# Kernel tuning notes

Hardware: AMD Instinct MI355X
Metric: run time of the kernel (lower is better)

Reference implementation:

```python
import jax, jax.numpy as jnp
import numpy as np

HIDDEN = 2048
N_HEADS = 16
N_KV = 2
HEAD_DIM = 256
PARTIAL = 0.25
ROT = int(HEAD_DIM * PARTIAL)  # 64
BATCH, SEQ = 1, 4096
NEG = -1e9


def apply_partial_rope(x, cos, sin):
    # x: (b, s, h, d); rotate first ROT dims (rotate-half convention), pass rest through.
    x_rot, x_pass = x[..., :ROT], x[..., ROT:]
    half = ROT // 2
    x1, x2 = x_rot[..., :half], x_rot[..., half:]
    c = cos[None, :, None, :]  # (1, s, 1, rot/2)
    s = sin[None, :, None, :]
    rotated = jnp.concatenate([x1 * c - x2 * s, x1 * s + x2 * c], axis=-1)
    return jnp.concatenate([rotated, x_pass], axis=-1)


def setup_inputs() -> dict:
    key = jax.random.key(0)
    ks = jax.random.split(key, 6)
    hidden_states = jax.random.normal(ks[0], (BATCH, SEQ, HIDDEN), dtype=jnp.float32)
    # RoPE tables: theta = 10000^{-2i/rot}
    inv_freq = 1.0 / (10000.0 ** (np.arange(0, ROT, 2, dtype=np.float32) / ROT))
    ang = np.arange(SEQ, dtype=np.float32)[:, None] * inv_freq[None, :]  # (s, rot/2)
    cos = jnp.asarray(np.cos(ang))
    sin = jnp.asarray(np.sin(ang))
    # causal mask (1,1,s,s)
    mask = jnp.triu(jnp.full((SEQ, SEQ), NEG, dtype=jnp.float32), k=1)[None, None]
    scale = 0.02
    wq = jax.random.normal(ks[1], (HIDDEN, N_HEADS * HEAD_DIM), dtype=jnp.float32) * scale
    wk = jax.random.normal(ks[2], (HIDDEN, N_KV * HEAD_DIM), dtype=jnp.float32) * scale
    wv = jax.random.normal(ks[3], (HIDDEN, N_KV * HEAD_DIM), dtype=jnp.float32) * scale
    wo = jax.random.normal(ks[4], (N_HEADS * HEAD_DIM, HIDDEN), dtype=jnp.float32) * scale
    return {"hidden_states": hidden_states, "cos": cos, "sin": sin,
            "attention_mask": mask, "wq": wq, "wk": wk, "wv": wv, "wo": wo}


def reference(hidden_states, cos, sin, attention_mask, wq, wk, wv, wo):
    b, s, _ = hidden_states.shape
    g = N_HEADS // N_KV
    scale = HEAD_DIM ** -0.5
    q = (hidden_states @ wq).reshape(b, s, N_HEADS, HEAD_DIM)
    k = (hidden_states @ wk).reshape(b, s, N_KV, HEAD_DIM)
    v = (hidden_states @ wv).reshape(b, s, N_KV, HEAD_DIM)
    q = apply_partial_rope(q, cos, sin)
    k = apply_partial_rope(k, cos, sin)
    new_k, new_v = k, v  # kv cache (no prior cache)
    # GQA without repeat_interleave: group q heads by their kv head.
    # repeat_interleave maps q head h -> kv head h // g, matching this reshape.
    qg = q.reshape(b, s, N_KV, g, HEAD_DIM)
    scores = jnp.einsum('bqkgd,blkd->bkgql', qg, k) * scale  # (b, kv, g, s, s)
    scores = scores + attention_mask[:, :, None]  # broadcast (b,1,1,s,s)
    probs = jax.nn.softmax(scores.astype(jnp.float32), axis=-1).astype(q.dtype)
    ctx = jnp.einsum('bkgql,blkd->bqkgd', probs, v)  # (b, s, kv, g, d)
    attn_out = ctx.reshape(b, s, N_HEADS * HEAD_DIM)
    output = attn_out @ wo
    return output, new_k, new_v
```

## Files before the change

### kernel.cpp

```cpp
#include <hip/hip_runtime.h>
#include <hip/hip_bf16.h>

typedef __bf16 bf16;
typedef bf16 bf16x8 __attribute__((ext_vector_type(8)));
typedef bf16 bf16x4 __attribute__((ext_vector_type(4)));
typedef float f32x4 __attribute__((ext_vector_type(4)));

#define SEQ    4096
#define HIDDEN 2048
#define NHEADS 16
#define NKV    2
#define HDIM   256
#define ROTD   64
#define ROTH   32
#define QN     (NHEADS*HDIM)
#define KVN    (NKV*HDIM)

typedef __attribute__((address_space(3))) unsigned int lds_u32;
typedef const __attribute__((address_space(1))) unsigned int glb_u32;
__device__ __forceinline__ void async_copy16(const void* g, void* l) {
  __builtin_amdgcn_global_load_lds((glb_u32*)g, (lds_u32*)l, 16, 0, 0);
}

__global__ __launch_bounds__(256) void convert_f32_bf16(
    const float* __restrict__ in, bf16* __restrict__ out, int n)
{
  int i = (blockIdx.x * 256 + threadIdx.x) * 4;
  if (i >= n) return;
  f32x4 v = *(const f32x4*)(in + i);
  bf16x4 o;
  #pragma unroll
  for (int j = 0; j < 4; j++) o[j] = (bf16)v[j];
  *(bf16x4*)(out + i) = o;
}

template<typename T>
__global__ __launch_bounds__(256) void transpose_to_bf16(
    const T* __restrict__ in, bf16* __restrict__ out, int R, int C)
{
  __shared__ float tile[32][33];
  int bx = blockIdx.x * 32;
  int by = blockIdx.y * 32;
  int tx = threadIdx.x & 31, ty = threadIdx.x >> 5;
  #pragma unroll
  for (int i = 0; i < 4; i++)
    tile[ty + i*8][tx] = (float)in[(size_t)(by + ty + i*8) * C + bx + tx];
  __syncthreads();
  #pragma unroll
  for (int i = 0; i < 4; i++)
    out[(size_t)(bx + ty + i*8) * R + by + tx] = (bf16)tile[tx][ty + i*8];
}

template<bool WF32, bool WBF16>
__global__ __launch_bounds__(256) void gemm_bt(
    const bf16* __restrict__ A, const bf16* __restrict__ Bt,
    float* __restrict__ Cf, bf16* __restrict__ Cb,
    int M, int N, int K)
{
  const int bm = blockIdx.y * 128;
  const int bn = blockIdx.x * 128;
  const int tid = threadIdx.x;
  const int wave = tid >> 6, lane = tid & 63;
  const int l16 = lane & 15, quad = lane >> 4;
  const int wr = (wave & 1) * 64;
  const int wc = (wave >> 1) * 64;

  __shared__ bf16 As[128*32];
  __shared__ bf16 Bs[128*32];

  f32x4 acc[4][4];
  #pragma unroll
  for (int r = 0; r < 4; r++)
    #pragma unroll
    for (int c = 0; c < 4; c++) acc[r][c] = (f32x4){0.f,0.f,0.f,0.f};

  const int arow = tid >> 2;
  const int acol = (tid & 3) * 8;
  const bf16* ag0 = A  + (size_t)(bm + arow)      * K + acol;
  const bf16* ag1 = A  + (size_t)(bm + 64 + arow) * K + acol;
  const bf16* bg0 = Bt + (size_t)(bn + arow)      * K + acol;
  const bf16* bg1 = Bt + (size_t)(bn + 64 + arow) * K + acol;
  bf16* la = As + tid*8;
  bf16* lb = Bs + tid*8;

  for (int kk = 0; kk < K; kk += 32) {
    __syncthreads();
    async_copy16(ag0 + kk, la);
    async_copy16(ag1 + kk, la + 2048);
    async_copy16(bg0 + kk, lb);
    async_copy16(bg1 + kk, lb + 2048);
    __syncthreads();

    bf16x8 af[4], bfr[4];
    #pragma unroll
    for (int r = 0; r < 4; r++) af[r]  = *(const bf16x8*)&As[(wr + r*16 + l16)*32 + quad*8];
    #pragma unroll
    for (int c = 0; c < 4; c++) bfr[c] = *(const bf16x8*)&Bs[(wc + c*16 + l16)*32 + quad*8];
    #pragma unroll
    for (int r = 0; r < 4; r++)
      #pragma unroll
      for (int c = 0; c < 4; c++)
        acc[r][c] = __builtin_amdgcn_mfma_f32_16x16x32_bf16(af[r], bfr[c], acc[r][c], 0, 0, 0);
  }

  #pragma unroll
  for (int r = 0; r < 4; r++)
    #pragma unroll
    for (int c = 0; c < 4; c++)
      #pragma unroll
      for (int rr = 0; rr < 4; rr++) {
        size_t idx = (size_t)(bm + wr + r*16 + quad*4 + rr) * N + bn + wc + c*16 + l16;
        if (WF32)  Cf[idx] = acc[r][c][rr];
        if (WBF16) Cb[idx] = (bf16)acc[r][c][rr];
      }
}

#define G256_STG(gp, stride, lbase, b, h, kt) do {                            \
    async_copy16((gp) + (size_t)((h)*128     ) * (stride) + (size_t)(kt)*64,  \
                 (lbase) + (b)*16384 + (h)*8192);                             \
    async_copy16((gp) + (size_t)((h)*128 + 64) * (stride) + (size_t)(kt)*64,  \
                 (lbase) + (b)*16384 + (h)*8192 + 4096);                      \
  } while (0)

#define G256_DSA(b, P) do {                                                   \
    _Pragma("unroll")                                                         \
    for (int m2 = 0; m2 < 2; m2++) {                                          \
      const int ro = (b)*16384 + arow0 + ((P)*2 + m2) * 1024;                 \
      af[m2][0] = *(const bf16x8*)&smem[ro + fc0];                            \
      af[m2][1] = *(const bf16x8*)&smem[ro + fc1];                            \
    }                                                                         \
  } while (0)

#define G256_DSB(b) do {                                                      \
    _Pragma("unroll")                                                         \
    for (int n4 = 0; n4 < 4; n4++) {                                          \
      const int ro = 32768 + (b)*16384 + brow0 + n4 * 1024;                   \
      bq[n4][0] = *(const bf16x8*)&smem[ro + fc0];                            \
      bq[n4][1] = *(const bf16x8*)&smem[ro + fc1];                            \
    }                                                                         \
  } while (0)

#define G256_MM(P) do {                                                       \
    _Pragma("unroll")                                                         \
    for (int m2 = 0; m2 < 2; m2++)                                            \
      _Pragma("unroll")                                                       \
      for (int n4 = 0; n4 < 4; n4++) {                                        \
        acc[(P)*2+m2][n4] = __builtin_amdgcn_mfma_f32_16x16x32_bf16(          \
            af[m2][0], bq[n4][0], acc[(P)*2+m2][n4], 0, 0, 0);                \
        acc[(P)*2+m2][n4] = __builtin_amdgcn_mfma_f32_16x16x32_bf16(          \
            af[m2][1], bq[n4][1], acc[(P)*2+m2][n4], 0, 0, 0);                \
      }                                                                       \
  } while (0)

#define G256_BAR  __builtin_amdgcn_s_barrier()
#define G256_WLG  do { asm volatile("s_waitcnt lgkmcnt(0)" ::: "memory");     \
                       __builtin_amdgcn_sched_barrier(0); } while (0)

template<bool WF32, bool WBF16>
__global__ __launch_bounds__(512, 2) void gemm256(
    const bf16* __restrict__ A, const bf16* __restrict__ Bt,
    float* __restrict__ Cf0, float* __restrict__ Cf1, bf16* __restrict__ Cb,
    int N, int K, int lda, int ldb)
{
  const int gx = gridDim.x;
  const int nwg = gx * gridDim.y;
  int wg = blockIdx.y * gx + blockIdx.x;
  wg = (wg & 7) * (nwg >> 3) + (wg >> 3);
  const int bn = (wg % gx) * 256;
  const int bm = (wg / gx) * 256;

  const int z = blockIdx.z;
  A  += (size_t)z * K;
  Bt += (size_t)z * K;
  float* __restrict__ Cf = z ? Cf1 : Cf0;

  const int tid = threadIdx.x;
  const int lane = tid & 63;
  const int l16 = lane & 15, quad = lane >> 4;
  const int wv = tid >> 6;
  const int wm = wv >> 2;
  const int wn = wv & 3;

  __shared__ bf16 smem[65536];

  const int srow = tid >> 3;
  const int scol = ((tid & 7) ^ (srow & 7)) << 3;
  const bf16* Ag = A  + (size_t)(bm + srow) * lda + scol;
  const bf16* Bg = Bt + (size_t)(bn + srow) * ldb + scol;
  bf16* lA = smem + tid * 8;
  bf16* lB = smem + 32768 + tid * 8;

  const int fsw = l16 & 7;
  const int fc0 = ((quad       ^ fsw) << 3);
  const int fc1 = (((4 + quad) ^ fsw) << 3);
  const int arow0 = (wm * 128 + l16) * 64;
  const int brow0 = (wn * 64  + l16) * 64;

  f32x4 acc[8][4];
  #pragma unroll
  for (int m = 0; m < 8; m++)
    #pragma unroll
    for (int n = 0; n < 4; n++) acc[m][n] = (f32x4){0.f,0.f,0.f,0.f};

  const int niter = K >> 7;

  G256_STG(Ag, lda, lA, 0, 0, 0);  G256_STG(Ag, lda, lA, 0, 1, 0);
  G256_STG(Bg, ldb, lB, 0, 0, 0);  G256_STG(Bg, ldb, lB, 0, 1, 0);
  G256_STG(Bg, ldb, lB, 1, 0, 1);  G256_STG(Bg, ldb, lB, 1, 1, 1);
  asm volatile("s_waitcnt vmcnt(4)" ::: "memory");
  G256_BAR;

  bf16x8 af[2][2];
  bf16x8 bq[4][2];

  for (int i = 0; i < niter; i++) {
    const int O = 2*i + 1;
    const bool nl = (i + 1 < niter);

    G256_DSB(0); G256_DSA(0, 0);
    G256_STG(Ag, lda, lA, 1, 0, O);
    G256_BAR; G256_WLG;
    __builtin_amdgcn_s_setprio(1); G256_MM(0); __builtin_amdgcn_s_setprio(0);
    G256_BAR;
    G256_DSA(0, 1);
    G256_STG(Ag, lda, lA, 1, 1, O);
    G256_BAR; G256_WLG;
    __builtin_amdgcn_s_setprio(1); G256_MM(1); __builtin_amdgcn_s_setprio(0);
    G256_BAR;
    G256_DSA(0, 2);
    if (nl) G256_STG(Bg, ldb, lB, 0, 0, O+1);
    G256_BAR; G256_WLG;
    __builtin_amdgcn_s_setprio(1); G256_MM(2); __builtin_amdgcn_s_setprio(0);
    G256_BAR;
    G256_DSA(0, 3);
    if (nl) G256_STG(Bg, ldb, lB, 0, 1, O+1);
    G256_BAR; G256_WLG;
    __builtin_amdgcn_s_setprio(1); G256_MM(3); __builtin_amdgcn_s_setprio(0);
    if (nl) asm volatile("s_waitcnt vmcnt(4)" ::: "memory");
    else    asm volatile("s_waitcnt vmcnt(0)" ::: "memory");
    G256_BAR;
    G256_DSB(1); G256_DSA(1, 0);
    if (nl) G256_STG(Ag, lda, lA, 0, 0, O+1);
    G256_BAR; G256_WLG;
    __builtin_amdgcn_s_setprio(1); G256_MM(0); __builtin_amdgcn_s_setprio(0);
    G256_BAR;
    G256_DSA(1, 1);
    if (nl) G256_STG(Ag, lda, lA, 0, 1, O+1);
    G256_BAR; G256_WLG;
    __builtin_amdgcn_s_setprio(1); G256_MM(1); __builtin_amdgcn_s_setprio(0);
    G256_BAR;
    G256_DSA(1, 2);
    if (nl) G256_STG(Bg, ldb, lB, 1, 0, O+2);
    G256_BAR; G256_WLG;
    __builtin_amdgcn_s_setprio(1); G256_MM(2); __builtin_amdgcn_s_setprio(0);
    G256_BAR;
    G256_DSA(1, 3);
    if (nl) G256_STG(Bg, ldb, lB, 1, 1, O+2);
    G256_BAR; G256_WLG;
    __builtin_amdgcn_s_setprio(1); G256_MM(3); __builtin_amdgcn_s_setprio(0);
    if (nl) asm volatile("s_waitcnt vmcnt(4)" ::: "memory");
    G256_BAR;
  }

  #pragma unroll
  for (int mf = 0; mf < 8; mf++)
    #pragma unroll
    for (int n = 0; n < 4; n++)
      #pragma unroll
      for (int rr = 0; rr < 4; rr++) {
        size_t idx = (size_t)(bm + wm*128 + mf*16 + quad*4 + rr) * N
                   + bn + wn*64 + n*16 + l16;
        if (WF32)  Cf[idx] = acc[mf][n][rr];
        if (WBF16) Cb[idx] = (bf16)acc[mf][n][rr];
      }
}

__global__ __launch_bounds__(256) void add_f32(
    const float* __restrict__ a, float* __restrict__ b, int n)
{
  int i = (blockIdx.x * 256 + threadIdx.x) * 4;
  if (i >= n) return;
  f32x4 x = *(const f32x4*)(a + i);
  f32x4 y = *(const f32x4*)(b + i);
  #pragma unroll
  for (int j = 0; j < 4; j++) y[j] += x[j];
  *(f32x4*)(b + i) = y;
}

__global__ __launch_bounds__(256) void rope_kernel(
    bf16* __restrict__ Q, bf16* __restrict__ K,
    const float* __restrict__ cosb, const float* __restrict__ sinb,
    float* __restrict__ newk)
{
  int s = blockIdx.x;
  int t = threadIdx.x;
  __shared__ float cf[ROTH], sf[ROTH];
  if (t < ROTH) { cf[t] = cosb[s*ROTH + t]; sf[t] = sinb[s*ROTH + t]; }
  __syncthreads();

  float qv[4];
  #pragma unroll
  for (int i = 0; i < 4; i++) {
    int w = t + 256*i;
    int h = w >> 6, d = w & 63;
    size_t base = ((size_t)s*NHEADS + h)*HDIM;
    if (d < ROTH) {
      float x1 = (float)Q[base + d], x2 = (float)Q[base + d + ROTH];
      qv[i] = x1*cf[d] - x2*sf[d];
    } else {
      int dd = d - ROTH;
      float x1 = (float)Q[base + dd], x2 = (float)Q[base + d];
      qv[i] = x1*sf[dd] + x2*cf[dd];
    }
  }
  float kvv[2];
  #pragma unroll
  for (int i = 0; i < 2; i++) {
    int w = t + 256*i;
    int h = w >> 8, d = w & 255;
    size_t base = ((size_t)s*NKV + h)*HDIM;
    if (d < ROTH) {
      kvv[i] = (float)K[base + d]*cf[d] - (float)K[base + d + ROTH]*sf[d];
    } else if (d < ROTD) {
      int dd = d - ROTH;
      kvv[i] = (float)K[base + dd]*sf[dd] + (float)K[base + d]*cf[dd];
    } else {
      kvv[i] = (float)K[base + d];
    }
  }
  __syncthreads();
  #pragma unroll
  for (int i = 0; i < 4; i++) {
    int w = t + 256*i;
    int h = w >> 6, d = w & 63;
    Q[((size_t)s*NHEADS + h)*HDIM + d] = (bf16)qv[i];
  }
  #pragma unroll
  for (int i = 0; i < 2; i++) {
    int w = t + 256*i;
    int h = w >> 8, d = w & 255;
    size_t base = ((size_t)s*NKV + h)*HDIM;
    K[base + d]    = (bf16)kvv[i];
    newk[base + d] = kvv[i];
  }
}

__global__ __launch_bounds__(256, 2) void attn_v5(
    const bf16* __restrict__ Q, const bf16* __restrict__ Kc,
    const bf16* __restrict__ Vt, bf16* __restrict__ ctx)
{
  const int h = blockIdx.y, kvh = h >> 3;
  const int qs = (int)(gridDim.x - 1 - blockIdx.x);
  const int tid = threadIdx.x, wave = tid >> 6, lane = tid & 63;
  const int l16 = lane & 15, quad = lane >> 4;
  const int q0 = qs*128 + wave*32;

  __shared__ bf16 Ks[32*256];
  __shared__ bf16 Vs[256*32];
  __shared__ bf16 PsAll[4][32][40];
  bf16 (*Ps)[40] = PsAll[wave];

  bf16x8 aq[2][8];
  #pragma unroll
  for (int u = 0; u < 2; u++) {
    const bf16* qp = Q + (size_t)(q0 + u*16 + l16)*QN + h*HDIM + quad*8;
    #pragma unroll
    for (int c = 0; c < 8; c++) aq[u][c] = *(const bf16x8*)(qp + c*32);
  }

  f32x4 o[2][16];
  #pragma unroll
  for (int u = 0; u < 2; u++)
    #pragma unroll
    for (int c = 0; c < 16; c++) o[u][c] = (f32x4){0.f,0.f,0.f,0.f};
  float lsum[2][4] = {{0.f,0.f,0.f,0.f},{0.f,0.f,0.f,0.f}};

  const int krow0 = tid >> 5;
  const int kcg   = ((tid & 31) ^ (krow0 & 7)) * 8;
  const bf16* kg  = Kc + (size_t)kvh*HDIM + kcg;
  const int vd0 = tid >> 2;
  const int vcg = ((tid & 3) ^ (vd0 & 3)) * 8;
  const bf16* vg  = Vt + (size_t)(kvh*HDIM + vd0)*SEQ + vcg;
  bf16* ksl = Ks + tid*8;
  bf16* vsl = Vs + tid*8;

  const int ntiles = qs*4 + 4;
  for (int t = 0; t < ntiles; t++) {
    const int l0 = t*32;
    __syncthreads();
    #pragma unroll
    for (int p = 0; p < 4; p++) {
      async_copy16(kg + (size_t)(l0 + p*8 + krow0)*KVN, ksl + p*2048);
      async_copy16(vg + (size_t)(p*64)*SEQ + l0,        vsl + p*2048);
    }
    __syncthreads();

    if (l0 > q0 + 31) continue;

    f32x4 s[2][2];
    #pragma unroll
    for (int u = 0; u < 2; u++)
      #pragma unroll
      for (int t4 = 0; t4 < 2; t4++) s[u][t4] = (f32x4){0.f,0.f,0.f,0.f};
    #pragma unroll
    for (int c = 0; c < 8; c++) {
      const int cs = ((c*4 + quad) ^ (l16 & 7)) * 8;
      #pragma unroll
      for (int t4 = 0; t4 < 2; t4++) {
        bf16x8 kb = *(const bf16x8*)&Ks[(t4*16 + l16)*256 + cs];
        #pragma unroll
        for (int u = 0; u < 2; u++)
          s[u][t4] = __builtin_amdgcn_mfma_f32_16x16x32_bf16(aq[u][c], kb, s[u][t4], 0, 0, 0);
      }
    }

    const bool need_mask = (l0 + 31 > q0);
    #pragma unroll
    for (int u = 0; u < 2; u++)
      #pragma unroll
      for (int r = 0; r < 4; r++) {
        const int row = q0 + u*16 + quad*4 + r;
        float p0 = __expf(fmaf(s[u][0][r], 0.0625f, -12.0f));
        float p1 = __expf(fmaf(s[u][1][r], 0.0625f, -12.0f));
        if (need_mask) {
          if (l0 +      l16 > row) p0 = 0.f;
          if (l0 + 16 + l16 > row) p1 = 0.f;
        }
        lsum[u][r] += p0 + p1;
        Ps[u*16 + quad*4 + r][l16]      = (bf16)p0;
        Ps[u*16 + quad*4 + r][16 + l16] = (bf16)p1;
      }

    bf16x8 pa[2];
    #pragma unroll
    for (int u = 0; u < 2; u++) pa[u] = *(const bf16x8*)&Ps[u*16 + l16][quad*8];
    #pragma unroll
    for (int c = 0; c < 16; c++) {
      const int vs = ((quad ^ (l16 & 3))) * 8;
      bf16x8 vb = *(const bf16x8*)&Vs[(c*16 + l16)*32 + vs];
      #pragma unroll
      for (int u = 0; u < 2; u++)
        o[u][c] = __builtin_amdgcn_mfma_f32_16x16x32_bf16(pa[u], vb, o[u][c], 0, 0, 0);
    }
  }

  #pragma unroll
  for (int u = 0; u < 2; u++)
    #pragma unroll
    for (int r = 0; r < 4; r++) {
      float l = lsum[u][r];
      l += __shfl_xor(l, 1);
      l += __shfl_xor(l, 2);
      l += __shfl_xor(l, 4);
      l += __shfl_xor(l, 8);
      float inv = 1.0f / l;
      size_t base = (size_t)(q0 + u*16 + quad*4 + r)*QN + h*HDIM;
      #pragma unroll
      for (int c = 0; c < 16; c++)
        ctx[base + c*16 + l16] = (bf16)(o[u][c][r] * inv);
    }
}

extern "C" void kernel_launch(void* const* d_in, const int* in_sizes, int n_in,
                              void* d_out, int out_size, void* d_ws, size_t ws_size,
                              hipStream_t stream)
{
  const float* X    = (const float*)d_in[0];
  const float* cosb = (const float*)d_in[1];
  const float* sinb = (const float*)d_in[2];
  const float* wq   = (const float*)d_in[4];
  const float* wk   = (const float*)d_in[5];
  const float* wv   = (const float*)d_in[6];
  const float* wo   = (const float*)d_in[7];

  float* out  = (float*)d_out;
  float* newk = out  + (size_t)SEQ*HIDDEN;
  float* newv = newk + (size_t)SEQ*KVN;

  bf16* Xb  = (bf16*)d_ws;
  bf16* wqT = Xb  + (size_t)SEQ*HIDDEN;
  bf16* Qb  = wqT + (size_t)QN*HIDDEN;
  bf16* Kb  = Qb  + (size_t)SEQ*QN;
  bf16* Vb  = Kb  + (size_t)SEQ*KVN;
  bf16* Vt  = Vb  + (size_t)SEQ*KVN;
  bf16* wkT = Vt  + (size_t)KVN*SEQ;
  bf16* wvT = wkT + (size_t)KVN*HIDDEN;
  bf16* woT = wvT + (size_t)KVN*HIDDEN;
  bf16* ctx = Xb;
  float* part = (float*)Qb;

  dim3 blk(256);
  convert_f32_bf16<<<dim3(SEQ*HIDDEN/1024), blk, 0, stream>>>(X, Xb, SEQ*HIDDEN);
  transpose_to_bf16<float><<<dim3(QN/32,     HIDDEN/32), blk, 0, stream>>>(wq, wqT, HIDDEN, QN);
  transpose_to_bf16<float><<<dim3(KVN/32,    HIDDEN/32), blk, 0, stream>>>(wk, wkT, HIDDEN, KVN);
  transpose_to_bf16<float><<<dim3(KVN/32,    HIDDEN/32), blk, 0, stream>>>(wv, wvT, HIDDEN, KVN);
  transpose_to_bf16<float><<<dim3(HIDDEN/32, QN/32),     blk, 0, stream>>>(wo, woT, QN, HIDDEN);

  gemm256<false,true><<<dim3(QN/256, SEQ/256, 1), dim3(512), 0, stream>>>(
      Xb, wqT, nullptr, nullptr, Qb, QN, HIDDEN, HIDDEN, HIDDEN);
  gemm_bt<false,true><<<dim3(KVN/128, SEQ/128), blk, 0, stream>>>(Xb, wkT, nullptr, Kb, SEQ, KVN, HIDDEN);
  gemm_bt<true, true><<<dim3(KVN/128, SEQ/128), blk, 0, stream>>>(Xb, wvT, newv,   Vb, SEQ, KVN, HIDDEN);

  rope_kernel<<<dim3(SEQ), blk, 0, stream>>>(Qb, Kb, cosb, sinb, newk);
  transpose_to_bf16<bf16><<<dim3(KVN/32, SEQ/32), blk, 0, stream>>>(Vb, Vt, SEQ, KVN);

  attn_v5<<<dim3(SEQ/128, NHEADS), blk, 0, stream>>>(Qb, Kb, Vt, ctx);

  gemm256<true,false><<<dim3(HIDDEN/256, SEQ/256, 2), dim3(512), 0, stream>>>(
      ctx, woT, out, part, nullptr, HIDDEN, QN/2, QN, QN);
  add_f32<<<dim3(SEQ*HIDDEN/1024), blk, 0, stream>>>(part, out, SEQ*HIDDEN);
}
```

Measured before the change: 741.3 us.

## Double-buffer K/V tiles in attention and reorder blocks for load balance

The attention kernel now keeps two LDS buffers for K and V and prefetches tile t+2 while tile t is being computed. Explicit vmcnt waits and barriers replace the two per-tile __syncthreads, which hides global-to-LDS latency behind the MFMA work. Blocks are also remapped so the long causal q-blocks are scheduled first and paired with short ones across the two halves of the grid, to balance work. The cost is double the K/V LDS footprint, which may reduce occupancy, plus hand-counted waitcnt logic that has to match the number of outstanding loads.

Result: faster. 722.6 us (-2.5%).

```diff
diff --git a/kernel.cpp b/kernel.cpp
--- a/kernel.cpp
+++ b/kernel.cpp
@@ -345,18 +345,20 @@
   }
 }
 
-__global__ __launch_bounds__(256, 2) void attn_v5(
+__global__ __launch_bounds__(256, 2) void attn_v6(
     const bf16* __restrict__ Q, const bf16* __restrict__ Kc,
     const bf16* __restrict__ Vt, bf16* __restrict__ ctx)
 {
-  const int h = blockIdx.y, kvh = h >> 3;
-  const int qs = (int)(gridDim.x - 1 - blockIdx.x);
+  const int d = blockIdx.y * gridDim.x + blockIdx.x;
+  const int r = (d < 256) ? d : 767 - d;
+  const int qs = 31 - (r >> 4);
+  const int h  = r & 15, kvh = h >> 3;
   const int tid = threadIdx.x, wave = tid >> 6, lane = tid & 63;
   const int l16 = lane & 15, quad = lane >> 4;
   const int q0 = qs*128 + wave*32;
 
-  __shared__ bf16 Ks[32*256];
-  __shared__ bf16 Vs[256*32];
+  __shared__ bf16 Ks[2][32*256];
+  __shared__ bf16 Vs[2][256*32];
   __shared__ bf16 PsAll[4][32][40];
   bf16 (*Ps)[40] = PsAll[wave];
 
@@ -381,83 +383,104 @@
   const int vd0 = tid >> 2;
   const int vcg = ((tid & 3) ^ (vd0 & 3)) * 8;
   const bf16* vg  = Vt + (size_t)(kvh*HDIM + vd0)*SEQ + vcg;
-  bf16* ksl = Ks + tid*8;
-  bf16* vsl = Vs + tid*8;
 
   const int ntiles = qs*4 + 4;
+
+  #define ATTN_STAGE(t, b) do {                                               \
+    const int _l0 = (t)*32;                                                   \
+    bf16* _ks = &Ks[b][0] + tid*8;                                            \
+    bf16* _vs = &Vs[b][0] + tid*8;                                            \
+    _Pragma("unroll")                                                         \
+    for (int p = 0; p < 4; p++) {                                             \
+      async_copy16(kg + (size_t)(_l0 + p*8 + krow0)*KVN, _ks + p*2048);       \
+      async_copy16(vg + (size_t)(p*64)*SEQ + _l0,        _vs + p*2048);       \
+    }                                                                         \
+  } while (0)
+
+  ATTN_STAGE(0, 0);
+  ATTN_STAGE(1, 1);
+  asm volatile("s_waitcnt vmcnt(8)" ::: "memory");
+  __builtin_amdgcn_s_barrier();
+
   for (int t = 0; t < ntiles; t++) {
+    const int b  = t & 1;
     const int l0 = t*32;
-    __syncthreads();
-    #pragma unroll
-    for (int p = 0; p < 4; p++) {
-      async_copy16(kg + (size_t)(l0 + p*8 + krow0)*KVN, ksl + p*2048);
-      async_copy16(vg + (size_t)(p*64)*SEQ + l0,        vsl + p*2048);
-    }
-    __syncthreads();
-
-    if (l0 > q0 + 31) continue;
-
-    f32x4 s[2][2];
-    #pragma unroll
-    for (int u = 0; u < 2; u++)
-      #pragma unroll
-      for (int t4 = 0; t4 < 2; t4++) s[u][t4] = (f32x4){0.f,0.f,0.f,0.f};
-    #pragma unroll
-    for (int c = 0; c < 8; c++) {
-      const int cs = ((c*4 + quad) ^ (l16 & 7)) * 8;
-      #pragma unroll
-      for (int t4 = 0; t4 < 2; t4++) {
-        bf16x8 kb = *(const bf16x8*)&Ks[(t4*16 + l16)*256 + cs];
+
+    if (l0 <= q0 + 31) {
+      f32x4 s[2][2];
+      #pragma unroll
+      for (int u = 0; u < 2; u++)
+        #pragma unroll
+        for (int t4 = 0; t4 < 2; t4++) s[u][t4] = (f32x4){0.f,0.f,0.f,0.f};
+      #pragma unroll
+      for (int c = 0; c < 8; c++) {
+        const int cs = ((c*4 + quad) ^ (l16 & 7)) * 8;
+        #pragma unroll
+        for (int t4 = 0; t4 < 2; t4++) {
+          bf16x8 kb = *(const bf16x8*)&Ks[b][(t4*16 + l16)*256 + cs];
+          #pragma unroll
+          for (int u = 0; u < 2; u++)
+            s[u][t4] = __builtin_amdgcn_mfma_f32_16x16x32_bf16(aq[u][c], kb, s[u][t4], 0, 0, 0);
+        }
+      }
+
+      const bool need_mask = (l0 + 31 > q0);
+      #pragma unroll
+      for (int u = 0; u < 2; u++)
+        #pragma unroll
+        for (int rr = 0; rr < 4; rr++) {
+          const int row = q0 + u*16 + quad*4 + rr;
+          float p0 = __expf(fmaf(s[u][0][rr], 0.0625f, -12.0f));
+          float p1 = __expf(fmaf(s[u][1][rr], 0.0625f, -12.0f));
+          if (need_mask) {
+            if (l0 +      l16 > row) p0 = 0.f;
+            if (l0 + 16 + l16 > row) p1 = 0.f;
+          }
+          lsum[u][rr] += p0 + p1;
+          Ps[u*16 + quad*4 + rr][l16]      = (bf16)p0;
+          Ps[u*16 + quad*4 + rr][16 + l16] = (bf16)p1;
+        }
+
+      bf16x8 pa[2];
+      #pragma unroll
+      for (int u = 0; u < 2; u++) pa[u] = *(const bf16x8*)&Ps[u*16 + l16][quad*8];
+      #pragma unroll
+      for (int c = 0; c < 16; c++) {
+        const int vs = ((quad ^ (l16 & 3))) * 8;
+        bf16x8 vb = *(const bf16x8*)&Vs[b][(c*16 + l16)*32 + vs];
         #pragma unroll
         for (int u = 0; u < 2; u++)
-          s[u][t4] = __builtin_amdgcn_mfma_f32_16x16x32_bf16(aq[u][c], kb, s[u][t4], 0, 0, 0);
+          o[u][c] = __builtin_amdgcn_mfma_f32_16x16x32_bf16(pa[u], vb, o[u][c], 0, 0, 0);
       }
     }
 
-    const bool need_mask = (l0 + 31 > q0);
-    #pragma unroll
-    for (int u = 0; u < 2; u++)
-      #pragma unroll
-      for (int r = 0; r < 4; r++) {
-        const int row = q0 + u*16 + quad*4 + r;
-        float p0 = __expf(fmaf(s[u][0][r], 0.0625f, -12.0f));
-        float p1 = __expf(fmaf(s[u][1][r], 0.0625f, -12.0f));
-        if (need_mask) {
-          if (l0 +      l16 > row) p0 = 0.f;
-          if (l0 + 16 + l16 > row) p1 = 0.f;
-        }
-        lsum[u][r] += p0 + p1;
-        Ps[u*16 + quad*4 + r][l16]      = (bf16)p0;
-        Ps[u*16 + quad*4 + r][16 + l16] = (bf16)p1;
+    if (t + 1 < ntiles) {
+      __builtin_amdgcn_s_barrier();
+      if (t + 2 < ntiles) {
+        ATTN_STAGE(t + 2, b);
+        asm volatile("s_waitcnt vmcnt(8)" ::: "memory");
+      } else {
+        asm volatile("s_waitcnt vmcnt(0)" ::: "memory");
       }
-
-    bf16x8 pa[2];
-    #pragma unroll
-    for (int u = 0; u < 2; u++) pa[u] = *(const bf16x8*)&Ps[u*16 + l16][quad*8];
-    #pragma unroll
-    for (int c = 0; c < 16; c++) {
-      const int vs = ((quad ^ (l16 & 3))) * 8;
-      bf16x8 vb = *(const bf16x8*)&Vs[(c*16 + l16)*32 + vs];
-      #pragma unroll
-      for (int u = 0; u < 2; u++)
-        o[u][c] = __builtin_amdgcn_mfma_f32_16x16x32_bf16(pa[u], vb, o[u][c], 0, 0, 0);
+      __builtin_amdgcn_s_barrier();
     }
   }
+  #undef ATTN_STAGE
 
   #pragma unroll
   for (int u = 0; u < 2; u++)
     #pragma unroll
-    for (int r = 0; r < 4; r++) {
-      float l = lsum[u][r];
+    for (int rr = 0; rr < 4; rr++) {
+      float l = lsum[u][rr];
       l += __shfl_xor(l, 1);
       l += __shfl_xor(l, 2);
       l += __shfl_xor(l, 4);
       l += __shfl_xor(l, 8);
       float inv = 1.0f / l;
-      size_t base = (size_t)(q0 + u*16 + quad*4 + r)*QN + h*HDIM;
+      size_t base = (size_t)(q0 + u*16 + quad*4 + rr)*QN + h*HDIM;
       #pragma unroll
       for (int c = 0; c < 16; c++)
-        ctx[base + c*16 + l16] = (bf16)(o[u][c][r] * inv);
+        ctx[base + c*16 + l16] = (bf16)(o[u][c][rr] * inv);
     }
 }
 
@@ -504,7 +527,7 @@
   rope_kernel<<<dim3(SEQ), blk, 0, stream>>>(Qb, Kb, cosb, sinb, newk);
   transpose_to_bf16<bf16><<<dim3(KVN/32, SEQ/32), blk, 0, stream>>>(Vb, Vt, SEQ, KVN);
 
-  attn_v5<<<dim3(SEQ/128, NHEADS), blk, 0, stream>>>(Qb, Kb, Vt, ctx);
+  attn_v6<<<dim3(SEQ/128, NHEADS), blk, 0, stream>>>(Qb, Kb, Vt, ctx);
 
   gemm256<true,false><<<dim3(HIDDEN/256, SEQ/256, 2), dim3(512), 0, stream>>>(
       ctx, woT, out, part, nullptr, HIDDEN, QN/2, QN, QN);
```
